# Kernel optimization log

Hardware: AMD Instinct MI355X
Metric: run time of the kernel (lower is better)

## Reference

```python
import jax, jax.numpy as jnp
import numpy as np

N, CIN, T, V = 32, 64, 256, 25
COUT = 192
K = 3                      # num_subset
INTER = COUT // 4          # coff_embedding = 4 -> 48
MID = COUT // 3            # 64
EPS = 1e-5


def _bn(x, g, b):
    # training-mode BatchNorm2d over (N, T, V) per channel
    m = x.mean(axis=(0, 2, 3), keepdims=True)
    v = x.var(axis=(0, 2, 3), keepdims=True)
    return (x - m) * jax.lax.rsqrt(v + EPS) * g[None, :, None, None] + b[None, :, None, None]


def _conv1x1(x, w, b):
    # w: [O, C]
    return jnp.einsum('oc,nctv->notv', w, x) + b[None, :, None, None]


def _tconv(x, w, b, pad):
    # w: [O, C, k, 1] temporal conv along T
    y = jax.lax.conv_general_dilated(x, w, (1, 1), ((pad, pad), (0, 0)),
                                     dimension_numbers=('NCHW', 'OIHW', 'NCHW'))
    return y + b[None, :, None, None]


def setup_inputs() -> dict:
    key = jax.random.key(0)
    ks = jax.random.split(key, 24)
    r = lambda i, shape, s=0.05: jax.random.normal(ks[i], shape, jnp.float32) * s
    return {
        'x': r(0, (N, CIN, T, V), 1.0),
        'A': jax.random.uniform(ks[1], (K, V, V), jnp.float32),   # fixed adjacency buffer
        'PA': jnp.full((K, V, V), 1e-6, jnp.float32),
        'Wa': r(2, (K, INTER, CIN)), 'ba': jnp.zeros((K, INTER), jnp.float32),
        'Wb': r(3, (K, INTER, CIN)), 'bb': jnp.zeros((K, INTER), jnp.float32),
        'Wd': r(4, (K, COUT, CIN)), 'bd': jnp.zeros((K, COUT), jnp.float32),
        'gcn_bn_g': jnp.ones(COUT, jnp.float32), 'gcn_bn_b': jnp.zeros(COUT, jnp.float32),
        'down_w': r(5, (COUT, CIN)), 'down_b': jnp.zeros(COUT, jnp.float32),
        'down_bn_g': jnp.ones(COUT, jnp.float32), 'down_bn_b': jnp.zeros(COUT, jnp.float32),
        'W11': r(6, (COUT, COUT)), 'b11': jnp.zeros(COUT, jnp.float32),
        'W21': r(7, (COUT, COUT)), 'b21': jnp.zeros(COUT, jnp.float32),
        'W31': r(8, (COUT, COUT)), 'b31': jnp.zeros(COUT, jnp.float32),
        'W12': r(9, (MID, COUT, 1, 1)), 'b12': jnp.zeros(MID, jnp.float32),
        'W22': r(10, (MID, COUT, 3, 1)), 'b22': jnp.zeros(MID, jnp.float32),
        'W32': r(11, (MID, COUT, 7, 1)), 'b32': jnp.zeros(MID, jnp.float32),
        'tcn_bn_g': jnp.ones(COUT, jnp.float32), 'tcn_bn_b': jnp.zeros(COUT, jnp.float32),
        'res_w': r(12, (COUT, CIN)), 'res_b': jnp.zeros(COUT, jnp.float32),
        'res_bn_g': jnp.ones(COUT, jnp.float32), 'res_bn_b': jnp.zeros(COUT, jnp.float32),
    }


def reference(x, A, PA, Wa, ba, Wb, bb, Wd, bd, gcn_bn_g, gcn_bn_b,
              down_w, down_b, down_bn_g, down_bn_b,
              W11, b11, W21, b21, W31, b31, W12, b12, W22, b22, W32, b32,
              tcn_bn_g, tcn_bn_b, res_w, res_b, res_bn_g, res_bn_b):
    n, c, t, v = x.shape
    # ---- unit_gcn (all num_subset branches vectorized over axis k) ----
    fa = jnp.einsum('kic,nctv->nkitv', Wa, x) + ba[None, :, :, None, None]
    fb = jnp.einsum('kic,nctv->nkitv', Wb, x) + bb[None, :, :, None, None]
    A1 = fa.transpose(0, 1, 4, 2, 3).reshape(n, K, v, INTER * t)   # [n,k,V,inter*T]
    A2 = fb.reshape(n, K, INTER * t, v)                            # [n,k,inter*T,V]
    scores = jnp.einsum('nkvd,nkdw->nkvw', A1, A2) / A1.shape[-1]
    att = jax.nn.softmax(scores, axis=-2) + (A + PA)[None]         # softmax over rows (dim -2)
    xv = x.reshape(n, c * t, v)
    z = jnp.einsum('ndv,nkvw->nkdw', xv, att).reshape(n, K, c, t, v)
    y = jnp.einsum('koc,nkctv->notv', Wd, z) + bd.sum(axis=0)[None, :, None, None]
    y = _bn(y, gcn_bn_g, gcn_bn_b)
    y = y + _bn(_conv1x1(x, down_w, down_b), down_bn_g, down_bn_b)
    g = jax.nn.relu(y)
    # ---- unit_tcn_m: three parallel (1x1 conv -> temporal conv) branches ----
    x1 = _tconv(_conv1x1(g, W11, b11), W12, b12, 0)
    x2 = _tconv(_conv1x1(g, W21, b21), W22, b22, 1)
    x3 = _tconv(_conv1x1(g, W31, b31), W32, b32, 3)
    tm = _bn(jnp.concatenate([x1, x2, x3], axis=1), tcn_bn_g, tcn_bn_b)
    # ---- residual: 1x1 unit_tcn on original input ----
    res = _bn(_conv1x1(x, res_w, res_b), res_bn_g, res_bn_b)
    return jax.nn.relu(tm + res)
```

## Files before the change

### kernel.cpp

```cpp
#include <hip/hip_runtime.h>
#include <hip/hip_bf16.h>
#include <cstdint>
#include <cstddef>

#define EPS_  1e-5f
#define NTV_  204800

typedef unsigned short u16;
typedef __attribute__((ext_vector_type(8))) short short8;
typedef __attribute__((ext_vector_type(4))) float f32x4;

__device__ __forceinline__ float bf2f(u16 u) {
  uint32_t x = (uint32_t)u << 16;
  float f;
  __builtin_memcpy(&f, &x, 4);
  return f;
}
__device__ __forceinline__ u16 f2bf(float f) {
  uint32_t x;
  __builtin_memcpy(&x, &f, 4);
  uint32_t r = (x + 0x7FFFu + ((x >> 16) & 1u)) >> 16;
  return (u16)r;
}

__device__ __forceinline__ void gload_lds16(const u16* g, u16* l) {
  __builtin_amdgcn_global_load_lds(
      (const __attribute__((address_space(1))) uint32_t*)g,
      (__attribute__((address_space(3))) uint32_t*)l, 16, 0, 0);
}

__global__ __launch_bounds__(256) void k_cvtw(
    const float* __restrict__ Wa, const float* __restrict__ Wb_,
    const float* __restrict__ dw, const float* __restrict__ rw,
    const float* __restrict__ Wd, const float* __restrict__ bd,
    const float* __restrict__ ba, const float* __restrict__ bb,
    const float* __restrict__ downbi, const float* __restrict__ resbi,
    u16* __restrict__ WB, float* __restrict__ bd2, float* __restrict__ fbias,
    float* __restrict__ cbias)
{
  int i = blockIdx.x * 256 + threadIdx.x;
  if (i < 9216) { WB[i] = f2bf(Wa[i]); return; }
  i -= 9216;
  if (i < 9216) { WB[9216 + i] = f2bf(Wb_[i]); return; }
  i -= 9216;
  if (i < 12288) { WB[18432 + i] = f2bf(dw[i]); return; }
  i -= 12288;
  if (i < 12288) { WB[30720 + i] = f2bf(rw[i]); return; }
  i -= 12288;
  if (i < 36864) {
    const int o = i / 192, r = i % 192, k = r >> 6, c = r & 63;
    WB[43008 + i] = f2bf(Wd[((size_t)(k * 192 + o)) * 64 + c]);
    return;
  }
  i -= 36864;
  if (i < 192) { bd2[i] = bd[i] + bd[192 + i] + bd[384 + i]; return; }
  i -= 192;
  if (i < 288) { fbias[i] = (i < 144) ? ba[i] : bb[i - 144]; return; }
  i -= 288;
  if (i < 384) {
    const int g = i / 192, o = i % 192;
    cbias[i] = (g == 0) ? downbi[o] : resbi[o];
  }
}

__global__ __launch_bounds__(256) void k_wcomp(
    const float* __restrict__ W11, const float* __restrict__ W21, const float* __restrict__ W31,
    const float* __restrict__ W12, const float* __restrict__ W22, const float* __restrict__ W32,
    const float* __restrict__ b11, const float* __restrict__ b21, const float* __restrict__ b31,
    u16* __restrict__ WC, float* __restrict__ btap)
{
  const int tapg = blockIdx.x;
  const int seg  = blockIdx.y;
  const float* W1; const float* W2; const float* b1; int tapl, KT;
  if (tapg == 0)      { W1 = W11; W2 = W12; b1 = b11; tapl = 0;        KT = 1; }
  else if (tapg < 4)  { W1 = W21; W2 = W22; b1 = b21; tapl = tapg - 1; KT = 3; }
  else                { W1 = W31; W2 = W32; b1 = b31; tapl = tapg - 4; KT = 7; }
  const int tid = threadIdx.x;
  const int idx = seg * 256 + tid;
  const int o = idx / 192, c = idx % 192;
  float s = 0.f;
#pragma unroll 4
  for (int m = 0; m < 192; ++m)
    s += W2[((size_t)o * 192 + m) * KT + tapl] * W1[(size_t)m * 192 + c];
  WC[(size_t)tapg * 12288 + idx] = f2bf(s);
  if (seg == 0 && tid < 64) {
    float sb = 0.f;
    for (int m = 0; m < 192; ++m)
      sb += W2[((size_t)tid * 192 + m) * KT + tapl] * b1[m];
    btap[tapg * 64 + tid] = sb;
  }
}

__global__ void k_bfull(const float* __restrict__ btap,
                        const float* __restrict__ b12, const float* __restrict__ b22,
                        const float* __restrict__ b32, float* __restrict__ bfull)
{
  const int tid = threadIdx.x;
  if (tid >= 192) return;
  const int br = tid / 64, o = tid % 64;
  float s = (br == 0) ? b12[o] : ((br == 1) ? b22[o] : b32[o]);
  const int t0 = (br == 0) ? 0 : ((br == 1) ? 1 : 4);
  const int kt = (br == 0) ? 1 : ((br == 1) ? 3 : 7);
  for (int tap = 0; tap < kt; ++tap) s += btap[(t0 + tap) * 64 + o];
  bfull[tid] = s;
}

__global__ __launch_bounds__(256) void k_xpose(const float* __restrict__ x, u16* __restrict__ xb)
{
  __shared__ u16 xt[256][72];
  const int bx = blockIdx.x;
  const int n = bx / 25, s0 = (bx % 25) * 256;
  const int tid = threadIdx.x;
  for (int l = tid; l < 64 * 64; l += 256) {
    const int c = l >> 6, q = l & 63;
    float4 v = *(const float4*)&x[((size_t)n * 64 + c) * 6400 + s0 + q * 4];
    xt[q * 4 + 0][c] = f2bf(v.x);
    xt[q * 4 + 1][c] = f2bf(v.y);
    xt[q * 4 + 2][c] = f2bf(v.z);
    xt[q * 4 + 3][c] = f2bf(v.w);
  }
  __syncthreads();
  for (int l = tid; l < 256 * 8; l += 256) {
    const int row = l >> 3, seg = l & 7;
    const int s_old = s0 + row;
    const int dv = s_old % 25, dt = s_old / 25;
    *(uint4*)&xb[((size_t)n * 6400 + dv * 256 + dt) * 64 + seg * 8] = *(const uint4*)&xt[row][seg * 8];
  }
}

template<int C, int NP, bool STATS>
__global__ __launch_bounds__(192) void k_conv5(
    const u16* __restrict__ in, const u16* __restrict__ Wb,
    const float* __restrict__ bias,
    u16* __restrict__ out0, u16* __restrict__ out1, u16* __restrict__ out2,
    float* __restrict__ stSum, float* __restrict__ stSq)
{
  constexpr int CS = C / 8;
  constexpr int CH = C / 32;
  constexpr int SB = 128 * CS;
  __shared__ u16 Bt[128 * C];
  __shared__ u16 Ep[3][16 * 72];

  const int bx = blockIdx.x;
  const int nb = bx / 50;
  const int sb = (bx % 50) * 128;
  const int tid = threadIdx.x;
  const int w = tid >> 6, lane = tid & 63;
  const int lr = lane & 15, lg = lane >> 4;

  for (int base = 0; base < SB; base += 192) {
    const int slot = base + tid;
    if ((SB % 192 == 0) || slot < SB) {
      const int r = slot / CS, q = slot % CS;
      gload_lds16(&in[((size_t)nb * 6400 + sb + r) * C + ((q ^ (r & 7)) << 3)],
                  &Bt[(size_t)(base + w * 64) * 8]);
    }
  }
  __syncthreads();

  u16* sc = Ep[w];
  const int o_w = w * 64;
  const int s0 = lane >> 3, seg = lane & 7;

  for (int p = 0; p < NP; ++p) {
    u16* outp = (p == 0) ? out0 : ((p == 1) ? out1 : out2);
    const u16* Ap = Wb + (size_t)p * 192 * C;
    short8 af[4][CH];
#pragma unroll
    for (int mi = 0; mi < 4; ++mi)
#pragma unroll
      for (int j = 0; j < CH; ++j)
        af[mi][j] = *(const short8*)&Ap[((size_t)(o_w + mi * 16 + lr)) * C + j * 32 + lg * 8];
    float4 bv[4];
#pragma unroll
    for (int mi = 0; mi < 4; ++mi)
      bv[mi] = *(const float4*)&bias[p * 192 + o_w + mi * 16 + lg * 4];
    float ssum[4][4] = {}, ssq[4][4] = {};

#pragma unroll
    for (int t = 0; t < 8; ++t) {
      f32x4 acc[4];
#pragma unroll
      for (int mi = 0; mi < 4; ++mi) {
        acc[mi][0] = 0.f; acc[mi][1] = 0.f; acc[mi][2] = 0.f; acc[mi][3] = 0.f;
      }
      const int rr = t * 16 + lr;
#pragma unroll
      for (int j = 0; j < CH; ++j) {
        short8 bf = *(const short8*)&Bt[((size_t)rr * CS + ((j * 4 + lg) ^ (rr & 7))) * 8];
#pragma unroll
        for (int mi = 0; mi < 4; ++mi)
          acc[mi] = __builtin_amdgcn_mfma_f32_16x16x32_bf16(af[mi][j], bf, acc[mi], 0, 0, 0);
      }
#pragma unroll
      for (int mi = 0; mi < 4; ++mi)
#pragma unroll
        for (int r = 0; r < 4; ++r) {
          float vv = acc[mi][r] + ((const float*)&bv[mi])[r];
          if (STATS) { ssum[mi][r] += vv; ssq[mi][r] += vv * vv; }
          sc[lr * 72 + mi * 16 + lg * 4 + r] = f2bf(vv);
        }
#pragma unroll
      for (int pass = 0; pass < 2; ++pass) {
        const int s = pass * 8 + s0;
        uint4 val = *(const uint4*)&sc[s * 72 + seg * 8];
        *(uint4*)&outp[((size_t)nb * 6400 + sb + t * 16 + s) * 192 + o_w + seg * 8] = val;
      }
    }

    if (STATS) {
#pragma unroll
      for (int mi = 0; mi < 4; ++mi)
#pragma unroll
        for (int r = 0; r < 4; ++r) {
          float ss = ssum[mi][r], sq = ssq[mi][r];
#pragma unroll
          for (int m = 1; m < 16; m <<= 1) { ss += __shfl_xor(ss, m); sq += __shfl_xor(sq, m); }
          if (lr == 0) {
            const int og = p * 192 + o_w + mi * 16 + lg * 4 + r;
            const int slot = bx & 15;
            atomicAdd(&stSum[og * 16 + slot], ss);
            atomicAdd(&stSq[og * 16 + slot], sq);
          }
        }
    }
  }
}

__global__ __launch_bounds__(256) void k_tconv12(
    const u16* __restrict__ g, const u16* __restrict__ WC,
    const float* __restrict__ bfull, const float* __restrict__ btap,
    u16* __restrict__ out, float* __restrict__ stSum, float* __restrict__ stSq,
    const u16* __restrict__ zp)
{
  constexpr int CS = 24, CH = 6;
  __shared__ u16 Bt[70 * 192];

  const int bx = blockIdx.x;
  const int nb = bx / 100;
  const int sb = (bx % 100) * 64;
  const int tbase = sb & 255;
  const int tid = threadIdx.x;
  const int w = tid >> 6, lane = tid & 63;
  const int lr = lane & 15, lg = lane >> 4;

  constexpr int SB = 70 * CS;
  for (int base = 0; base < SB; base += 256) {
    const int slot = base + tid;
    if (slot < SB) {
      const int r = slot / CS, q = slot % CS;
      const int t = tbase - 3 + r;
      const u16* src = ((unsigned)t < 256u)
          ? &g[((size_t)nb * 6400 + sb - 3 + r) * 192 + ((q ^ (r & 7)) << 3)]
          : zp;
      gload_lds16(src, &Bt[(size_t)(base + w * 64) * 8]);
    }
  }
  __syncthreads();

  const bool edge = (tbase == 0) || (tbase == 192);

  for (int br = 0; br < 3; ++br) {
    const int KT = (br == 0) ? 1 : ((br == 1) ? 3 : 7);
    const int tb0 = (br == 0) ? 0 : ((br == 1) ? 1 : 4);
    const u16* Wp = WC + (size_t)tb0 * 12288;

    f32x4 acc[4];
#pragma unroll
    for (int t = 0; t < 4; ++t) {
      acc[t][0] = 0.f; acc[t][1] = 0.f; acc[t][2] = 0.f; acc[t][3] = 0.f;
    }
    const int hofs = 3 - KT / 2;
    for (int tap = 0; tap < KT; ++tap) {
      short8 af[CH];
#pragma unroll
      for (int j = 0; j < CH; ++j)
        af[j] = *(const short8*)&Wp[((size_t)(tap * 64 + w * 16 + lr)) * 192 + j * 32 + lg * 8];
#pragma unroll
      for (int t = 0; t < 4; ++t) {
        const int rr = t * 16 + lr + hofs + tap;
#pragma unroll
        for (int j = 0; j < CH; ++j) {
          short8 bf = *(const short8*)&Bt[((size_t)rr * CS + ((j * 4 + lg) ^ (rr & 7))) * 8];
          acc[t] = __builtin_amdgcn_mfma_f32_16x16x32_bf16(af[j], bf, acc[t], 0, 0, 0);
        }
      }
    }

    float bb[4];
    {
      const float4 bv = *(const float4*)&bfull[br * 64 + w * 16 + lg * 4];
      bb[0] = bv.x; bb[1] = bv.y; bb[2] = bv.z; bb[3] = bv.w;
    }
    float ssum[4] = {}, ssq[4] = {};
#pragma unroll
    for (int t = 0; t < 4; ++t) {
      float b4[4] = {bb[0], bb[1], bb[2], bb[3]};
      if (KT > 1 && edge) {
        const int trow = tbase + t * 16 + lr;
        for (int tap = 0; tap < KT; ++tap) {
          const int dt = tap - KT / 2;
          if ((unsigned)(trow + dt) >= 256u) {
            const float4 bv = *(const float4*)&btap[(tb0 + tap) * 64 + w * 16 + lg * 4];
            b4[0] -= bv.x; b4[1] -= bv.y; b4[2] -= bv.z; b4[3] -= bv.w;
          }
        }
      }
      union { uint2 u; u16 s[4]; } pk;
#pragma unroll
      for (int r = 0; r < 4; ++r) {
        float vv = acc[t][r] + b4[r];
        ssum[r] += vv; ssq[r] += vv * vv;
        pk.s[r] = f2bf(vv);
      }
      *(uint2*)&out[((size_t)nb * 6400 + sb + t * 16 + lr) * 192 +
                    br * 64 + w * 16 + lg * 4] = pk.u;
    }
#pragma unroll
    for (int r = 0; r < 4; ++r) {
      float ss = ssum[r], sq = ssq[r];
#pragma unroll
      for (int m = 1; m < 16; m <<= 1) { ss += __shfl_xor(ss, m); sq += __shfl_xor(sq, m); }
      if (lr == 0) {
        const int og = br * 64 + w * 16 + lg * 4 + r;
        const int slot = bx & 15;
        atomicAdd(&stSum[og * 16 + slot], ss);
        atomicAdd(&stSq[og * 16 + slot], sq);
      }
    }
  }
}

__global__ __launch_bounds__(256) void k_gemm_cf(
    const u16* __restrict__ in, const u16* __restrict__ Wb,
    const float* __restrict__ bias, u16* __restrict__ out)
{
  __shared__ u16 Bt[128 * 64];
  __shared__ u16 At[288 * 64];
  __shared__ u16 SC[48 * 136];

  const int bx = blockIdx.x;
  const int nb = bx / 50;
  const int sb = (bx % 50) * 128;
  const int v = sb >> 8, tbase = sb & 255;
  const int tid = threadIdx.x;
  const int w = tid >> 6, lane = tid & 63;
  const int lr = lane & 15, lg = lane >> 4;
  const int s_w = w * 32;

  for (int base = 0; base < 1024; base += 256) {
    const int slot = base + tid;
    const int r = slot >> 3, q = slot & 7;
    gload_lds16(&in[((size_t)nb * 6400 + v * 256 + tbase + r) * 64 + ((q ^ (r & 7)) << 3)],
                &Bt[(size_t)(base + w * 64) * 8]);
  }
  for (int base = 0; base < 2304; base += 256) {
    const int slot = base + tid;
    const int r = slot >> 3, q = slot & 7;
    gload_lds16(&Wb[(size_t)r * 64 + ((q ^ (r & 7)) << 3)],
                &At[(size_t)(base + w * 64) * 8]);
  }
  __syncthreads();

  for (int p = 0; p < 6; ++p) {
    f32x4 acc[3][2];
#pragma unroll
    for (int mi = 0; mi < 3; ++mi)
#pragma unroll
      for (int ni = 0; ni < 2; ++ni) {
        acc[mi][ni][0] = 0.f; acc[mi][ni][1] = 0.f; acc[mi][ni][2] = 0.f; acc[mi][ni][3] = 0.f;
      }
#pragma unroll
    for (int ch = 0; ch < 2; ++ch) {
      const int j = ch * 4 + lg;
      short8 af[3], bf[2];
#pragma unroll
      for (int mi = 0; mi < 3; ++mi) {
        const int r = p * 48 + mi * 16 + lr;
        af[mi] = *(const short8*)&At[((size_t)r * 8 + (j ^ (r & 7))) * 8];
      }
#pragma unroll
      for (int ni = 0; ni < 2; ++ni) {
        const int r = s_w + ni * 16 + lr;
        bf[ni] = *(const short8*)&Bt[((size_t)r * 8 + (j ^ (r & 7))) * 8];
      }
#pragma unroll
      for (int mi = 0; mi < 3; ++mi)
#pragma unroll
        for (int ni = 0; ni < 2; ++ni)
          acc[mi][ni] = __builtin_amdgcn_mfma_f32_16x16x32_bf16(af[mi], bf[ni], acc[mi][ni], 0, 0, 0);
    }
#pragma unroll
    for (int mi = 0; mi < 3; ++mi)
#pragma unroll
      for (int r = 0; r < 4; ++r) {
        const float bv = bias[p * 48 + mi * 16 + lg * 4 + r];
#pragma unroll
        for (int ni = 0; ni < 2; ++ni) acc[mi][ni][r] += bv;
      }
    __syncthreads();
#pragma unroll
    for (int mi = 0; mi < 3; ++mi)
#pragma unroll
      for (int ni = 0; ni < 2; ++ni)
#pragma unroll
        for (int r = 0; r < 4; ++r)
          SC[(mi * 16 + lg * 4 + r) * 136 + s_w + ni * 16 + lr] = f2bf(acc[mi][ni][r]);
    __syncthreads();
#pragma unroll
    for (int it = 0; it < 3; ++it) {
      const int row = it * 16 + (tid >> 4), chunk = tid & 15;
      *(uint4*)&out[((size_t)nb * 288 + p * 48 + row) * 6400 + sb + chunk * 8] =
          *(const uint4*)&SC[row * 136 + chunk * 8];
    }
  }
}

__device__ __forceinline__ float dot4(uint2 a, uint2 b) {
  return bf2f((u16)(a.x & 0xffff)) * bf2f((u16)(b.x & 0xffff)) +
         bf2f((u16)(a.x >> 16))    * bf2f((u16)(b.x >> 16)) +
         bf2f((u16)(a.y & 0xffff)) * bf2f((u16)(b.y & 0xffff)) +
         bf2f((u16)(a.y >> 16))    * bf2f((u16)(b.y >> 16));
}

__global__ __launch_bounds__(256) void k_scores_part(
    const u16* __restrict__ fab, float* __restrict__ part)
{
  const int nk = blockIdx.x;
  const int seg = blockIdx.y;
  const int n = nk / 3, k = nk % 3;
  __shared__ u16 sa[12800], sb[12800];
  const int tid = threadIdx.x;
  const u16* fap = fab + ((size_t)(n * 288 + k * 48 + seg * 2)) * 6400;
  const u16* fbp = fab + ((size_t)(n * 288 + 144 + k * 48 + seg * 2)) * 6400;
  for (int l = tid; l < 1600; l += 256) {
    ((uint4*)sa)[l] = ((const uint4*)fap)[l];
    ((uint4*)sb)[l] = ((const uint4*)fbp)[l];
  }
  __syncthreads();

  const int l0 = tid, l1 = tid + 256, l2 = tid + 512;
  const bool ok2 = (l2 < 625);
  const int v0 = l0 / 25, w0 = l0 % 25;
  const int v1 = l1 / 25, w1 = l1 % 25;
  const int v2 = ok2 ? l2 / 25 : 0, w2 = ok2 ? l2 % 25 : 0;
  float a0 = 0.f, a1 = 0.f, a2 = 0.f;
  const int rot = ((tid & 63) * 4) & 255;

#pragma unroll
  for (int ch = 0; ch < 2; ++ch) {
    const u16* pa = sa + ch * 6400;
    const u16* pb = sb + ch * 6400;
    for (int it = 0; it < 64; ++it) {
      const int t = (it * 4 + rot) & 255;
      a0 += dot4(*(const uint2*)&pa[v0 * 256 + t], *(const uint2*)&pb[w0 * 256 + t]);
      a1 += dot4(*(const uint2*)&pa[v1 * 256 + t], *(const uint2*)&pb[w1 * 256 + t]);
      if (ok2)
        a2 += dot4(*(const uint2*)&pa[v2 * 256 + t], *(const uint2*)&pb[w2 * 256 + t]);
    }
  }
  float* po = part + ((size_t)nk * 24 + seg) * 640;
  po[l0] = a0;
  po[l1] = a1;
  if (ok2) po[l2] = a2;
}

__global__ __launch_bounds__(256) void k_softmax(
    const float* __restrict__ part, const float* __restrict__ A,
    const float* __restrict__ PA, float* __restrict__ att)
{
  const int nk = blockIdx.x;
  const int n = nk / 3, k = nk % 3;
  __shared__ float sc[640];
  const int tid = threadIdx.x;
  const float* pb = part + (size_t)nk * 24 * 640;
  for (int l = tid; l < 625; l += 256) {
    float s = 0.f;
#pragma unroll
    for (int seg = 0; seg < 24; ++seg) s += pb[seg * 640 + l];
    sc[l] = s;
  }
  __syncthreads();
  if (tid < 25) {
    const int w = tid;
    const float scale = 1.f / 12288.f;
    float m = -1e30f;
    for (int v = 0; v < 25; ++v) m = fmaxf(m, sc[v * 25 + w]);
    m *= scale;
    float e[25], sum = 0.f;
#pragma unroll
    for (int v = 0; v < 25; ++v) { e[v] = __expf(sc[v * 25 + w] * scale - m); sum += e[v]; }
    const float inv = 1.f / sum;
    const float* Ak = A + k * 625;
    const float* Pk = PA + k * 625;
    float* ao = att + ((size_t)n * 3 + k) * 625;
#pragma unroll
    for (int v = 0; v < 25; ++v) ao[v * 25 + w] = e[v] * inv + Ak[v * 25 + w] + Pk[v * 25 + w];
  }
}

__global__ __launch_bounds__(256) void k_z(
    const u16* __restrict__ xb, const float* __restrict__ att, u16* __restrict__ z)
{
  __shared__ float attl[1950];
  __shared__ u16 xt[12800];
  const int bx = blockIdx.x;
  const int n = bx >> 5, tb = (bx & 31) * 8;
  const int tid = threadIdx.x;

  for (int l = tid; l < 1875; l += 256) {
    const int k = l / 625, vw = l % 625, v = vw / 25, w = vw % 25;
    attl[(k * 25 + v) * 26 + w] = att[((size_t)n * 3 + k) * 625 + vw];
  }
  for (int l = tid; l < 200 * 8; l += 256) {
    const int j = l >> 3, seg = l & 7;
    const int vv = j >> 3, tl = j & 7;
    *(uint4*)&xt[j * 64 + seg * 8] =
        *(const uint4*)&xb[((size_t)n * 6400 + vv * 256 + tb + tl) * 64 + seg * 8];
  }
  __syncthreads();

  for (int it = 0; it < 19; ++it) {
    const int l = tid + it * 256;
    if (l >= 4800) break;
    const int hi = l >> 6, lo = l & 63;
    const int k = hi / 25, w = hi % 25;
    const int tl = lo >> 3, c0 = (lo & 7) * 8;
    float accv[8] = {};
    for (int v = 0; v < 25; ++v) {
      const float aw = attl[(k * 25 + v) * 26 + w];
      union { uint4 u; u16 s[8]; } xv;
      xv.u = *(const uint4*)&xt[(v * 8 + tl) * 64 + c0];
#pragma unroll
      for (int jj = 0; jj < 8; ++jj) accv[jj] += aw * bf2f(xv.s[jj]);
    }
    union { uint4 u; u16 s[8]; } ov;
#pragma unroll
    for (int jj = 0; jj < 8; ++jj) ov.s[jj] = f2bf(accv[jj]);
    *(uint4*)&z[((size_t)n * 6400 + w * 256 + tb + tl) * 192 + k * 64 + c0] = ov.u;
  }
}

__global__ void k_bnparams(const float* __restrict__ sSum, const float* __restrict__ sSq,
                           const float* __restrict__ gamma, const float* __restrict__ beta,
                           float* __restrict__ a, float* __restrict__ c, int O)
{
  const int o = threadIdx.x + blockIdx.x * blockDim.x;
  if (o >= O) return;
  float sum = 0.f, sq = 0.f;
#pragma unroll
  for (int s = 0; s < 16; ++s) { sum += sSum[o * 16 + s]; sq += sSq[o * 16 + s]; }
  const float mean = sum * (1.f / NTV_);
  const float var = sq * (1.f / NTV_) - mean * mean;
  const float inv = rsqrtf(var + EPS_);
  const float av = gamma[o] * inv;
  a[o] = av;
  c[o] = beta[o] - av * mean;
}

__global__ __launch_bounds__(256) void k_g2(
    const u16* __restrict__ ypre, const u16* __restrict__ down,
    const float* __restrict__ ga, const float* __restrict__ gc,
    const float* __restrict__ da, const float* __restrict__ dc,
    u16* __restrict__ g)
{
  __shared__ float pA1[192], pC1[192], pA2[192], pC2[192];
  const int tid = threadIdx.x;
  if (tid < 192) { pA1[tid] = ga[tid]; pC1[tid] = gc[tid]; pA2[tid] = da[tid]; pC2[tid] = dc[tid]; }
  __syncthreads();
  for (size_t i8 = (size_t)blockIdx.x * 256 + tid; i8 < 4915200; i8 += (size_t)gridDim.x * 256) {
    const int c0 = (int)(i8 % 24) * 8;
    union { uint4 u; u16 s[8]; } yv, dv, ov;
    yv.u = *(const uint4*)&ypre[i8 * 8];
    dv.u = *(const uint4*)&down[i8 * 8];
#pragma unroll
    for (int j = 0; j < 8; ++j) {
      const int c = c0 + j;
      ov.s[j] = f2bf(fmaxf(pA1[c] * bf2f(yv.s[j]) + pC1[c] + pA2[c] * bf2f(dv.s[j]) + pC2[c], 0.f));
    }
    *(uint4*)&g[i8 * 8] = ov.u;
  }
}

__global__ __launch_bounds__(256) void k_out(
    const u16* __restrict__ tm, const u16* __restrict__ resp,
    const float* __restrict__ ta, const float* __restrict__ tc,
    const float* __restrict__ ra, const float* __restrict__ rc,
    float* __restrict__ out)
{
  __shared__ u16 L[100][200];
  __shared__ float pA1[192], pC1[192], pA2[192], pC2[192];
  const int bx = blockIdx.x;
  const int n = bx >> 6, t0 = (bx & 63) * 4;
  const int tid = threadIdx.x;
  if (tid < 192) { pA1[tid] = ta[tid]; pC1[tid] = tc[tid]; pA2[tid] = ra[tid]; pC2[tid] = rc[tid]; }
  __syncthreads();
  for (int l = tid; l < 2400; l += 256) {
    const int row = l / 24, ch = l % 24;
    const int v = row >> 2, tl = row & 3;
    const size_t src = ((size_t)n * 6400 + v * 256 + t0 + tl) * 192 + ch * 8;
    union { uint4 u; u16 s[8]; } tv, rv;
    tv.u = *(const uint4*)&tm[src];
    rv.u = *(const uint4*)&resp[src];
#pragma unroll
    for (int j = 0; j < 8; ++j) {
      const int c = ch * 8 + j;
      L[row][c] = f2bf(fmaxf(pA1[c] * bf2f(tv.s[j]) + pC1[c] + pA2[c] * bf2f(rv.s[j]) + pC2[c], 0.f));
    }
  }
  __syncthreads();
  for (int j = tid; j < 192 * 25; j += 256) {
    const int o = j / 25, q = j % 25;
    float4 f4;
#pragma unroll
    for (int e = 0; e < 4; ++e) {
      const int idx = q * 4 + e;
      const int tl = idx / 25, v = idx % 25;
      ((float*)&f4)[e] = bf2f(L[v * 4 + tl][o]);
    }
    *(float4*)&out[((size_t)n * 192 + o) * 6400 + t0 * 25 + q * 4] = f4;
  }
}

extern "C" void kernel_launch(void* const* d_in, const int* in_sizes, int n_in,
                              void* d_out, int out_size, void* d_ws, size_t ws_size,
                              hipStream_t stream)
{
  const float* x      = (const float*)d_in[0];
  const float* A      = (const float*)d_in[1];
  const float* PA     = (const float*)d_in[2];
  const float* Wa     = (const float*)d_in[3];
  const float* ba     = (const float*)d_in[4];
  const float* Wb     = (const float*)d_in[5];
  const float* bb     = (const float*)d_in[6];
  const float* Wd     = (const float*)d_in[7];
  const float* bd     = (const float*)d_in[8];
  const float* gcng   = (const float*)d_in[9];
  const float* gcnb   = (const float*)d_in[10];
  const float* downw  = (const float*)d_in[11];
  const float* downbi = (const float*)d_in[12];
  const float* downg  = (const float*)d_in[13];
  const float* downb  = (const float*)d_in[14];
  const float* W11    = (const float*)d_in[15];
  const float* b11    = (const float*)d_in[16];
  const float* W21    = (const float*)d_in[17];
  const float* b21    = (const float*)d_in[18];
  const float* W31    = (const float*)d_in[19];
  const float* b31    = (const float*)d_in[20];
  const float* W12    = (const float*)d_in[21];
  const float* b12    = (const float*)d_in[22];
  const float* W22    = (const float*)d_in[23];
  const float* b22    = (const float*)d_in[24];
  const float* W32    = (const float*)d_in[25];
  const float* b32    = (const float*)d_in[26];
  const float* tcng   = (const float*)d_in[27];
  const float* tcnb   = (const float*)d_in[28];
  const float* resw   = (const float*)d_in[29];
  const float* resbi  = (const float*)d_in[30];
  const float* resg   = (const float*)d_in[31];
  const float* resb   = (const float*)d_in[32];
  (void)in_sizes; (void)n_in; (void)out_size; (void)ws_size;

  u16* ob = (u16*)d_out;
  u16* fab   = ob;
  u16* xb    = ob + 58982400;
  float* att = (float*)(ob + 72089600);
  float* part  = (float*)(ob + 72584768);
  float* fbias = (float*)(ob + 75533888);
  u16*   WC    = ob + 75534464;
  float* btap  = (float*)(ob + 75669760);
  float* bfull = (float*)(ob + 75671296);

  char* ws = (char*)d_ws;
  const size_t SLOT = 78643200;
  u16* z     = (u16*)(ws);
  u16* g     = (u16*)(ws);
  u16* ypre  = (u16*)(ws + SLOT);
  u16* down  = (u16*)(ws + 2 * SLOT);
  u16* tm    = (u16*)(ws + 2 * SLOT);
  u16* resp  = (u16*)(ws + 3 * SLOT);
  char* sm   = ws + 4 * SLOT;
  float* bnp   = (float*)(sm);
  u16*   zp    = (u16*)(sm + 8192);
  u16*   WB    = (u16*)(sm + 8704);
  float* bd2   = (float*)(sm + 660224);
  float* cbias = (float*)(sm + 661248);
  float* slots = (float*)(sm + 665600);
  float* gcnSum = slots;           float* gcnSq = slots + 3072;
  float* dwnSum = slots + 6144;    float* resSum = slots + 9216;
  float* dwnSq  = slots + 12288;   float* resSq  = slots + 15360;
  float* tmSum  = slots + 18432;   float* tmSq   = slots + 21504;
  float* gcnA = bnp;          float* gcnC = bnp + 192;
  float* dwnA = bnp + 384;    float* dwnC = bnp + 576;
  float* resA = bnp + 768;    float* resC = bnp + 960;
  float* tmA  = bnp + 1152;   float* tmC  = bnp + 1344;

  hipMemsetAsync(slots, 0, 24576 * 4, stream);
  hipMemsetAsync(zp, 0, 256, stream);

  const dim3 blk(256);
  const dim3 blk3(192);

  k_cvtw<<<dim3(316), blk, 0, stream>>>(Wa, Wb, downw, resw, Wd, bd, ba, bb,
                                        downbi, resbi, WB, bd2, fbias, cbias);
  k_wcomp<<<dim3(11, 48), blk, 0, stream>>>(W11, W21, W31, W12, W22, W32,
                                            b11, b21, b31, WC, btap);
  k_bfull<<<dim3(1), dim3(192), 0, stream>>>(btap, b12, b22, b32, bfull);
  k_xpose<<<dim3(800), blk, 0, stream>>>(x, xb);

  k_gemm_cf<<<dim3(1600), blk, 0, stream>>>(xb, WB, fbias, fab);
  k_scores_part<<<dim3(96, 24), blk, 0, stream>>>(fab, part);
  k_softmax<<<dim3(96), blk, 0, stream>>>(part, A, PA, att);
  k_z<<<dim3(1024), blk, 0, stream>>>(xb, att, z);
  k_conv5<192, 1, true><<<dim3(1600), blk3, 0, stream>>>(
      z, WB + 43008, bd2, ypre, ypre, ypre, gcnSum, gcnSq);
  k_conv5<64, 2, true><<<dim3(1600), blk3, 0, stream>>>(
      xb, WB + 18432, cbias, down, resp, resp, dwnSum, dwnSq);
  k_bnparams<<<dim3(1), dim3(192), 0, stream>>>(gcnSum, gcnSq, gcng, gcnb, gcnA, gcnC, 192);
  k_bnparams<<<dim3(1), dim3(192), 0, stream>>>(dwnSum, dwnSq, downg, downb, dwnA, dwnC, 192);
  k_bnparams<<<dim3(1), dim3(192), 0, stream>>>(resSum, resSq, resg, resb, resA, resC, 192);
  k_g2<<<dim3(2048), blk, 0, stream>>>(ypre, down, gcnA, gcnC, dwnA, dwnC, g);

  k_tconv12<<<dim3(3200), blk, 0, stream>>>(
      g, WC, bfull, btap, tm, tmSum, tmSq, zp);
  k_bnparams<<<dim3(1), dim3(192), 0, stream>>>(tmSum, tmSq, tcng, tcnb, tmA, tmC, 192);

  k_out<<<dim3(2048), blk, 0, stream>>>(tm, resp, tmA, tmC, resA, resC, (float*)d_out);
}
```

Baseline: 761.3 us.

## Retile 1x1 conv kernel to 64-row blocks with four waves and direct stores

The 1x1 conv GEMM kernel now handles 64 spatial rows per block with 256 threads instead of 128 rows with 192 threads, doubling the grid. Each wave covers 16 output channels per 64-channel branch and loops over three branches, loading one weight fragment set at a time. The LDS staging of the epilogue is dropped: results are packed and written straight to global memory as 8-byte stores. This cuts LDS and register use to raise occupancy and parallelism, at the cost of reloading weights per branch, smaller uncoalesced stores, and twice as many stat atomics.

Measured after the change: 901.0 us. 18.3% more time.

```diff
diff --git a/kernel.cpp b/kernel.cpp
--- a/kernel.cpp
+++ b/kernel.cpp
@@ -129,7 +129,7 @@
 }
 
 template<int C, int NP, bool STATS>
-__global__ __launch_bounds__(192) void k_conv5(
+__global__ __launch_bounds__(256) void k_conv7(
     const u16* __restrict__ in, const u16* __restrict__ Wb,
     const float* __restrict__ bias,
     u16* __restrict__ out0, u16* __restrict__ out1, u16* __restrict__ out2,
@@ -137,92 +137,77 @@
 {
   constexpr int CS = C / 8;
   constexpr int CH = C / 32;
-  constexpr int SB = 128 * CS;
-  __shared__ u16 Bt[128 * C];
-  __shared__ u16 Ep[3][16 * 72];
+  __shared__ u16 Bt[64 * C];
 
   const int bx = blockIdx.x;
-  const int nb = bx / 50;
-  const int sb = (bx % 50) * 128;
+  const int nb = bx / 100;
+  const int sb = (bx % 100) * 64;
   const int tid = threadIdx.x;
   const int w = tid >> 6, lane = tid & 63;
   const int lr = lane & 15, lg = lane >> 4;
 
-  for (int base = 0; base < SB; base += 192) {
+  constexpr int SB = 64 * CS;
+#pragma unroll
+  for (int base = 0; base < SB; base += 256) {
     const int slot = base + tid;
-    if ((SB % 192 == 0) || slot < SB) {
-      const int r = slot / CS, q = slot % CS;
-      gload_lds16(&in[((size_t)nb * 6400 + sb + r) * C + ((q ^ (r & 7)) << 3)],
-                  &Bt[(size_t)(base + w * 64) * 8]);
-    }
-  }
-  __syncthreads();
-
-  u16* sc = Ep[w];
-  const int o_w = w * 64;
-  const int s0 = lane >> 3, seg = lane & 7;
+    const int r = slot / CS, q = slot % CS;
+    gload_lds16(&in[((size_t)nb * 6400 + sb + r) * C + ((q ^ (r & 7)) << 3)],
+                &Bt[(size_t)(base + w * 64) * 8]);
+  }
+  __syncthreads();
 
   for (int p = 0; p < NP; ++p) {
     u16* outp = (p == 0) ? out0 : ((p == 1) ? out1 : out2);
-    const u16* Ap = Wb + (size_t)p * 192 * C;
-    short8 af[4][CH];
-#pragma unroll
-    for (int mi = 0; mi < 4; ++mi)
+    for (int br = 0; br < 3; ++br) {
+      const u16* Ap = Wb + ((size_t)p * 192 + br * 64) * C;
+      short8 af[CH];
 #pragma unroll
       for (int j = 0; j < CH; ++j)
-        af[mi][j] = *(const short8*)&Ap[((size_t)(o_w + mi * 16 + lr)) * C + j * 32 + lg * 8];
-    float4 bv[4];
-#pragma unroll
-    for (int mi = 0; mi < 4; ++mi)
-      bv[mi] = *(const float4*)&bias[p * 192 + o_w + mi * 16 + lg * 4];
-    float ssum[4][4] = {}, ssq[4][4] = {};
-
-#pragma unroll
-    for (int t = 0; t < 8; ++t) {
+        af[j] = *(const short8*)&Ap[((size_t)(w * 16 + lr)) * C + j * 32 + lg * 8];
+
       f32x4 acc[4];
 #pragma unroll
-      for (int mi = 0; mi < 4; ++mi) {
-        acc[mi][0] = 0.f; acc[mi][1] = 0.f; acc[mi][2] = 0.f; acc[mi][3] = 0.f;
-      }
-      const int rr = t * 16 + lr;
-#pragma unroll
-      for (int j = 0; j < CH; ++j) {
-        short8 bf = *(const short8*)&Bt[((size_t)rr * CS + ((j * 4 + lg) ^ (rr & 7))) * 8];
-#pragma unroll
-        for (int mi = 0; mi < 4; ++mi)
-          acc[mi] = __builtin_amdgcn_mfma_f32_16x16x32_bf16(af[mi][j], bf, acc[mi], 0, 0, 0);
-      }
-#pragma unroll
-      for (int mi = 0; mi < 4; ++mi)
+      for (int t = 0; t < 4; ++t) {
+        acc[t][0] = 0.f; acc[t][1] = 0.f; acc[t][2] = 0.f; acc[t][3] = 0.f;
+      }
+#pragma unroll
+      for (int t = 0; t < 4; ++t) {
+        const int rr = t * 16 + lr;
+#pragma unroll
+        for (int j = 0; j < CH; ++j) {
+          short8 bf = *(const short8*)&Bt[((size_t)rr * CS + ((j * 4 + lg) ^ (rr & 7))) * 8];
+          acc[t] = __builtin_amdgcn_mfma_f32_16x16x32_bf16(af[j], bf, acc[t], 0, 0, 0);
+        }
+      }
+
+      const float4 bv4 = *(const float4*)&bias[p * 192 + br * 64 + w * 16 + lg * 4];
+      float ssum[4] = {}, ssq[4] = {};
+#pragma unroll
+      for (int t = 0; t < 4; ++t) {
+        union { uint2 u; u16 s[4]; } pk;
 #pragma unroll
         for (int r = 0; r < 4; ++r) {
-          float vv = acc[mi][r] + ((const float*)&bv[mi])[r];
-          if (STATS) { ssum[mi][r] += vv; ssq[mi][r] += vv * vv; }
-          sc[lr * 72 + mi * 16 + lg * 4 + r] = f2bf(vv);
+          float vv = acc[t][r] + ((const float*)&bv4)[r];
+          if (STATS) { ssum[r] += vv; ssq[r] += vv * vv; }
+          pk.s[r] = f2bf(vv);
         }
-#pragma unroll
-      for (int pass = 0; pass < 2; ++pass) {
-        const int s = pass * 8 + s0;
-        uint4 val = *(const uint4*)&sc[s * 72 + seg * 8];
-        *(uint4*)&outp[((size_t)nb * 6400 + sb + t * 16 + s) * 192 + o_w + seg * 8] = val;
-      }
-    }
-
-    if (STATS) {
-#pragma unroll
-      for (int mi = 0; mi < 4; ++mi)
+        *(uint2*)&outp[((size_t)nb * 6400 + sb + t * 16 + lr) * 192 +
+                       br * 64 + w * 16 + lg * 4] = pk.u;
+      }
+      if (STATS) {
 #pragma unroll
         for (int r = 0; r < 4; ++r) {
-          float ss = ssum[mi][r], sq = ssq[mi][r];
+          float ss = ssum[r], sq = ssq[r];
 #pragma unroll
           for (int m = 1; m < 16; m <<= 1) { ss += __shfl_xor(ss, m); sq += __shfl_xor(sq, m); }
           if (lr == 0) {
-            const int og = p * 192 + o_w + mi * 16 + lg * 4 + r;
+            const int og = p * 192 + br * 64 + w * 16 + lg * 4 + r;
             const int slot = bx & 15;
             atomicAdd(&stSum[og * 16 + slot], ss);
             atomicAdd(&stSq[og * 16 + slot], sq);
           }
         }
+      }
     }
   }
 }
@@ -699,7 +684,6 @@
   hipMemsetAsync(zp, 0, 256, stream);
 
   const dim3 blk(256);
-  const dim3 blk3(192);
 
   k_cvtw<<<dim3(316), blk, 0, stream>>>(Wa, Wb, downw, resw, Wd, bd, ba, bb,
                                         downbi, resbi, WB, bd2, fbias, cbias);
@@ -712,9 +696,9 @@
   k_scores_part<<<dim3(96, 24), blk, 0, stream>>>(fab, part);
   k_softmax<<<dim3(96), blk, 0, stream>>>(part, A, PA, att);
   k_z<<<dim3(1024), blk, 0, stream>>>(xb, att, z);
-  k_conv5<192, 1, true><<<dim3(1600), blk3, 0, stream>>>(
+  k_conv7<192, 1, true><<<dim3(3200), blk, 0, stream>>>(
       z, WB + 43008, bd2, ypre, ypre, ypre, gcnSum, gcnSq);
-  k_conv5<64, 2, true><<<dim3(1600), blk3, 0, stream>>>(
+  k_conv7<64, 2, true><<<dim3(3200), blk, 0, stream>>>(
       xb, WB + 18432, cbias, down, resp, resp, dwnSum, dwnSq);
   k_bnparams<<<dim3(1), dim3(192), 0, stream>>>(gcnSum, gcnSq, gcng, gcnb, gcnA, gcnC, 192);
   k_bnparams<<<dim3(1), dim3(192), 0, stream>>>(dwnSum, dwnSq, downg, downb, dwnA, dwnC, 192);
```
